# Optimization experiments

Measured on AMD Instinct MI355X. Metric: run time of the kernel, lower is better.

The kernel has to match this reference:

```python
import jax, jax.numpy as jnp
import numpy as np
from jax import lax

# mamba-130m-style config
B, L = 2, 1024          # batch, seq_len
D = 768                 # hidden_size
E = 1536                # intermediate (expand=2)
N = 16                  # ssm state size
R = 48                  # time_step_rank = ceil(D/16)
K = 4                   # conv kernel
NL = 4                  # num layers
NC = 5                  # num classes
EPS = 1e-5


def setup_inputs() -> dict:
    key = jax.random.key(0)
    ks = jax.random.split(key, 10)
    s = 0.02
    return {
        "x": jax.random.normal(ks[0], (B, L, 12), dtype=jnp.float32),
        "proj_w": jax.random.normal(ks[1], (D, 12)) * s,
        "proj_b": jnp.zeros((D,), jnp.float32),
        "norm_w": jnp.ones((NL, D), jnp.float32),
        "in_w": jax.random.normal(ks[2], (NL, 2 * E, D)) * s,
        "conv_w": jax.random.normal(ks[3], (NL, E, K)) * s,
        "conv_b": jnp.zeros((NL, E), jnp.float32),
        "xproj_w": jax.random.normal(ks[4], (NL, R + 2 * N, E)) * s,
        "dt_w": jax.random.normal(ks[5], (NL, E, R)) * s,
        "dt_b": jnp.full((NL, E), -4.0, jnp.float32),  # softplus(-4) ~ small dt
        "A_log": jnp.tile(jnp.log(jnp.arange(1, N + 1, dtype=jnp.float32))[None, None, :], (NL, E, 1)),
        "D_param": jnp.ones((NL, E), jnp.float32),
        "out_w": jax.random.normal(ks[6], (NL, D, E)) * s,
        "fnorm_w": jnp.ones((D,), jnp.float32),
        "cls_w": jax.random.normal(ks[7], (NC, D)) * s,
        "cls_b": jnp.zeros((NC,), jnp.float32),
    }


def _rmsnorm(x, w):
    var = jnp.mean(x * x, axis=-1, keepdims=True)
    return x * lax.rsqrt(var + EPS) * w


def _causal_conv(u, w, b):
    # u: [B,L,E], w: [E,K] depthwise causal conv, left-pad K-1
    up = jnp.pad(u, ((0, 0), (K - 1, 0), (0, 0)))
    y = b
    for k in range(K):
        y = y + w[:, k] * up[:, k:k + L, :]
    return y


def _selective_scan(u, dt, A, Bm, Cm, Dp):
    # u, dt: [B,L,E]; Bm, Cm: [B,L,N]; A: [E,N]; Dp: [E]
    def step(h, inp):
        u_t, dt_t, B_t, C_t = inp  # [B,E],[B,E],[B,N],[B,N]
        dA = jnp.exp(dt_t[:, :, None] * A)                      # [B,E,N]
        h = h * dA + dt_t[:, :, None] * B_t[:, None, :] * u_t[:, :, None]
        y = jnp.einsum('ben,bn->be', h, C_t)
        return h, y

    h0 = jnp.zeros((u.shape[0], E, N), u.dtype)
    _, ys = lax.scan(step, h0,
                     (u.transpose(1, 0, 2), dt.transpose(1, 0, 2),
                      Bm.transpose(1, 0, 2), Cm.transpose(1, 0, 2)))
    return ys.transpose(1, 0, 2) + u * Dp


def reference(x, proj_w, proj_b, norm_w, in_w, conv_w, conv_b, xproj_w,
              dt_w, dt_b, A_log, D_param, out_w, fnorm_w, cls_w, cls_b):
    h = x @ proj_w.T + proj_b                                     # [B,L,D]
    for i in range(NL):
        res = h
        hn = _rmsnorm(h, norm_w[i])
        proj = hn @ in_w[i].T                                     # [B,L,2E]
        u, gate = proj[..., :E], proj[..., E:]
        u = jax.nn.silu(_causal_conv(u, conv_w[i], conv_b[i]))    # [B,L,E]
        xdbc = u @ xproj_w[i].T                                   # [B,L,R+2N]
        dt_r = xdbc[..., :R]
        Bm = xdbc[..., R:R + N]
        Cm = xdbc[..., R + N:]
        dt = jax.nn.softplus(dt_r @ dt_w[i].T + dt_b[i])          # [B,L,E]
        A = -jnp.exp(A_log[i])                                    # [E,N]
        y = _selective_scan(u, dt, A, Bm, Cm, D_param[i])
        y = y * jax.nn.silu(gate)
        h = res + y @ out_w[i].T
    h = _rmsnorm(h, fnorm_w)
    pooled = jnp.mean(h, axis=1)                                  # AdaptiveAvgPool1d(1)
    return pooled @ cls_w.T + cls_b                               # [B,NC]
```

## Files before the change

kernel.cpp:

```cpp
#include <hip/hip_runtime.h>

constexpr int B_  = 2;
constexpr int L_  = 1024;
constexpr int D_  = 768;
constexpr int E_  = 1536;
constexpr int N_  = 16;
constexpr int R_  = 48;
constexpr int NL_ = 4;
constexpr int NC_ = 5;
constexpr int M_  = B_ * L_;
constexpr int E2_ = 2 * E_;
constexpr int XD_ = R_ + 2 * N_;
constexpr float EPS_ = 1e-5f;

constexpr int NCH_ = 16;
constexpr int CL_  = L_ / NCH_;
constexpr int KS_  = 8;
constexpr int PC_  = 64;

typedef __attribute__((ext_vector_type(8))) short bf16x8;
typedef __attribute__((ext_vector_type(4))) float f32x4;
typedef const __attribute__((address_space(1))) void* gas_t;
typedef __attribute__((address_space(3))) void* las_t;

__device__ __forceinline__ float sigm(float x) { return 1.0f / (1.0f + __expf(-x)); }
__device__ __forceinline__ float softplusf(float x) { return x > 20.0f ? x : log1pf(__expf(x)); }
__device__ __forceinline__ ushort f2b(float f) {
  union { float f; unsigned u; } v; v.f = f;
  unsigned r = (v.u + 0x7fffu + ((v.u >> 16) & 1u)) >> 16;
  return (ushort)r;
}
__device__ __forceinline__ float b2f(ushort u) {
  union { unsigned u; float f; } v; v.u = ((unsigned)u) << 16;
  return v.f;
}
__device__ __forceinline__ float b2f_lo(unsigned p) {
  union { unsigned u; float f; } v; v.u = p << 16;
  return v.f;
}
__device__ __forceinline__ float b2f_hi(unsigned p) {
  union { unsigned u; float f; } v; v.u = p & 0xffff0000u;
  return v.f;
}

template <int CTRL>
__device__ __forceinline__ float dpp_add(float x) {
  int yi = __builtin_amdgcn_update_dpp(0, __builtin_bit_cast(int, x), CTRL, 0xf, 0xf, false);
  return x + __builtin_bit_cast(float, yi);
}
__device__ __forceinline__ float row_sum16(float x) {
  x = dpp_add<0x121>(x);
  x = dpp_add<0x122>(x);
  x = dpp_add<0x124>(x);
  x = dpp_add<0x128>(x);
  return x;
}

__device__ __forceinline__ float block_sum(float v, float* sm) {
  #pragma unroll
  for (int o = 32; o > 0; o >>= 1) v += __shfl_xor(v, o);
  if ((threadIdx.x & 63) == 0) sm[threadIdx.x >> 6] = v;
  __syncthreads();
  return sm[0] + sm[1] + sm[2] + sm[3];
}

constexpr int WS1_ = NL_ * E2_ * D_;
constexpr int WS2_ = NL_ * D_ * E_;
constexpr int WS3_ = NL_ * XD_ * E_;
constexpr int WS4_ = NL_ * E_ * 64;
constexpr int WTOT_ = WS1_ + WS2_ + WS3_ + WS4_;
constexpr int WB_ = WTOT_ / 4 / 256;
__global__ __launch_bounds__(256) void k_wprep(const float* __restrict__ in_w, const float* __restrict__ out_w,
                                               const float* __restrict__ xw, const float* __restrict__ dw,
                                               const float* __restrict__ nw,
                                               ushort* __restrict__ in_wb, ushort* __restrict__ out_wb,
                                               ushort* __restrict__ xwb, ushort* __restrict__ dtwb,
                                               const float* __restrict__ x, const float* __restrict__ pw,
                                               const float* __restrict__ pb, float* __restrict__ h,
                                               ushort* __restrict__ hb, float* __restrict__ ssq) {
  if (blockIdx.x >= WB_) {
    __shared__ float xs[12];
    __shared__ float sm[4];
    int bx = blockIdx.x - WB_;
    int m = bx / 3;
    int d = (bx % 3) * 256 + threadIdx.x;
    if (threadIdx.x < 12) xs[threadIdx.x] = x[m * 12 + threadIdx.x];
    __syncthreads();
    float acc = pb[d];
    #pragma unroll
    for (int j = 0; j < 12; j++) acc = fmaf(xs[j], pw[d * 12 + j], acc);
    h[(size_t)m * D_ + d] = acc;
    hb[(size_t)m * D_ + d] = f2b(acc);
    float s = block_sum(acc * acc, sm);
    if (threadIdx.x == 0) atomicAdd(&ssq[m], s);
    return;
  }
  int i = (blockIdx.x * 256 + threadIdx.x) * 4;
  if (i < WS1_) {
    float4 v = *(const float4*)(in_w + i);
    int l = i / (E2_ * D_);
    int d = i % D_;
    float4 w = *(const float4*)(nw + l * D_ + d);
    *(ushort4*)(in_wb + i) = make_ushort4(f2b(v.x * w.x), f2b(v.y * w.y), f2b(v.z * w.z), f2b(v.w * w.w));
  } else if (i < WS1_ + WS2_) {
    int j = i - WS1_;
    float4 v = *(const float4*)(out_w + j);
    *(ushort4*)(out_wb + j) = make_ushort4(f2b(v.x), f2b(v.y), f2b(v.z), f2b(v.w));
  } else if (i < WS1_ + WS2_ + WS3_) {
    int j = i - WS1_ - WS2_;
    float4 v = *(const float4*)(xw + j);
    *(ushort4*)(xwb + j) = make_ushort4(f2b(v.x), f2b(v.y), f2b(v.z), f2b(v.w));
  } else {
    int j = i - WS1_ - WS2_ - WS3_;
    int k = j & 63, e = j >> 6;
    ushort4 o;
    o.x = (k + 0 < R_) ? f2b(dw[e * R_ + k + 0]) : (ushort)0;
    o.y = (k + 1 < R_) ? f2b(dw[e * R_ + k + 1]) : (ushort)0;
    o.z = (k + 2 < R_) ? f2b(dw[e * R_ + k + 2]) : (ushort)0;
    o.w = (k + 3 < R_) ? f2b(dw[e * R_ + k + 3]) : (ushort)0;
    *(ushort4*)(dtwb + j) = o;
  }
}

template <int BM, int BN, int MODE>
__global__ __launch_bounds__(256) void k_gemm_bf(const ushort* __restrict__ A, const ushort* __restrict__ Bw,
                                                 void* __restrict__ Cv, const float* __restrict__ res,
                                                 ushort* __restrict__ Cb, float* __restrict__ ssq,
                                                 int Kd, int Nd) {
  constexpr int AM = BM / 32, BNF = BN / 32;
  __shared__ ushort sA[BM * 32];
  __shared__ ushort sB[BN * 32];
  const int tid = threadIdx.x;
  const int wave = tid >> 6, lane = tid & 63;
  const int q = lane >> 4, r = lane & 15;
  const int wm = wave >> 1, wn = wave & 1;
  const int m0 = blockIdx.y * BM, n0 = blockIdx.x * BN;
  f32x4 acc[AM][BNF] = {};

  for (int k0 = 0; k0 < Kd; k0 += 32) {
    #pragma unroll
    for (int j = 0; j < BM / 64; j++) {
      int i = j * 256 + tid;
      const ushort* gp = A + (size_t)(m0 + (i >> 2)) * Kd + k0 + ((i & 3) << 3);
      __builtin_amdgcn_global_load_lds((gas_t)gp, (las_t)(sA + ((j * 256 + wave * 64) << 3)), 16, 0, 0);
    }
    #pragma unroll
    for (int j = 0; j < BN / 64; j++) {
      int i = j * 256 + tid;
      const ushort* gp = Bw + (size_t)(n0 + (i >> 2)) * Kd + k0 + ((i & 3) << 3);
      __builtin_amdgcn_global_load_lds((gas_t)gp, (las_t)(sB + ((j * 256 + wave * 64) << 3)), 16, 0, 0);
    }
    __syncthreads();
    bf16x8 af[AM], bfv[BNF];
    #pragma unroll
    for (int mi = 0; mi < AM; mi++)
      af[mi] = *(const bf16x8*)&sA[(wm * (BM / 2) + mi * 16 + r) * 32 + q * 8];
    #pragma unroll
    for (int nj = 0; nj < BNF; nj++)
      bfv[nj] = *(const bf16x8*)&sB[(wn * (BN / 2) + nj * 16 + r) * 32 + q * 8];
    #pragma unroll
    for (int mi = 0; mi < AM; mi++)
      #pragma unroll
      for (int nj = 0; nj < BNF; nj++)
        acc[mi][nj] = __builtin_amdgcn_mfma_f32_16x16x32_bf16(af[mi], bfv[nj], acc[mi][nj], 0, 0, 0);
    __syncthreads();
  }
  #pragma unroll
  for (int mi = 0; mi < AM; mi++) {
    #pragma unroll
    for (int rg = 0; rg < 4; rg++) {
      int row = m0 + wm * (BM / 2) + mi * 16 + q * 4 + rg;
      float rs = 0.0f, ssl = 0.0f;
      if (MODE == 4) rs = rsqrtf(res[row] * (1.0f / D_) + EPS_);
      #pragma unroll
      for (int nj = 0; nj < BNF; nj++) {
        int col = n0 + wn * (BN / 2) + nj * 16 + r;
        size_t off = (size_t)row * Nd + col;
        float v = acc[mi][nj][rg];
        if (MODE == 4) {
          ((ushort*)Cv)[off] = f2b(v * rs);
        } else if (MODE == 5) {
          v += res[off];
          ((float*)Cv)[off] = v;
          Cb[off] = f2b(v);
          ssl = fmaf(v, v, ssl);
        }
      }
      if (MODE == 5) {
        float sr = row_sum16(ssl);
        if (r == 0) atomicAdd(&ssq[row], sr);
      }
    }
  }
}

__global__ __launch_bounds__(256) void k_gemm_x(const ushort* __restrict__ A, const ushort* __restrict__ Bw,
                                                float* __restrict__ part) {
  __shared__ ushort sA[64 * 32];
  __shared__ ushort sB[80 * 32];
  const int tid = threadIdx.x;
  const int wave = tid >> 6, lane = tid & 63;
  const int q = lane >> 4, r = lane & 15;
  const int m0 = blockIdx.x * 64;
  const int kbeg = blockIdx.y * (E_ / KS_), kend = kbeg + E_ / KS_;
  f32x4 acc[5] = {};

  for (int k0 = kbeg; k0 < kend; k0 += 32) {
    {
      const ushort* gp = A + (size_t)(m0 + wave * 16 + (lane >> 2)) * E_ + k0 + ((lane & 3) << 3);
      __builtin_amdgcn_global_load_lds((gas_t)gp, (las_t)(sA + (wave << 9)), 16, 0, 0);
    }
    #pragma unroll
    for (int j = wave; j < 5; j += 4) {
      const ushort* gp = Bw + (size_t)(j * 16 + (lane >> 2)) * E_ + k0 + ((lane & 3) << 3);
      __builtin_amdgcn_global_load_lds((gas_t)gp, (las_t)(sB + (j << 9)), 16, 0, 0);
    }
    __syncthreads();
    bf16x8 af = *(const bf16x8*)&sA[(wave * 16 + r) * 32 + q * 8];
    #pragma unroll
    for (int nj = 0; nj < 5; nj++) {
      bf16x8 bfv = *(const bf16x8*)&sB[(nj * 16 + r) * 32 + q * 8];
      acc[nj] = __builtin_amdgcn_mfma_f32_16x16x32_bf16(af, bfv, acc[nj], 0, 0, 0);
    }
    __syncthreads();
  }
  float* pp = part + (size_t)blockIdx.y * M_ * XD_;
  #pragma unroll
  for (int nj = 0; nj < 5; nj++) {
    int col = nj * 16 + r;
    #pragma unroll
    for (int rg = 0; rg < 4; rg++) {
      int row = m0 + wave * 16 + q * 4 + rg;
      pp[(size_t)row * XD_ + col] = acc[nj][rg];
    }
  }
}

__global__ __launch_bounds__(256) void k_xfin(const float* __restrict__ part, float* __restrict__ xdbc,
                                              ushort* __restrict__ xb, float* __restrict__ ssq) {
  int i = blockIdx.x * 256 + threadIdx.x;
  if (i < M_) ssq[i] = 0.0f;
  int m = i / XD_, col = i - m * XD_;
  float s = 0.0f;
  #pragma unroll
  for (int ks = 0; ks < KS_; ks++) s += part[(size_t)ks * M_ * XD_ + i];
  xdbc[i] = s;
  if (col < R_) xb[(size_t)m * 64 + col] = f2b(s);
  else if (col < 64) xb[(size_t)m * 64 + col] = 0;
}

constexpr int TC_ = 4;
__global__ __launch_bounds__(384) void k_conv2(const ushort* __restrict__ proj, const float* __restrict__ cw,
                                               const float* __restrict__ cb, ushort* __restrict__ ub16,
                                               ushort* __restrict__ gb16) {
  int m0 = blockIdx.x * TC_;
  int t0 = m0 & (L_ - 1);
  int base = m0 - t0;
  int e4 = threadIdx.x * 4;
  float wv[4][4];
  #pragma unroll
  for (int j = 0; j < 4; j++) {
    float4 w = *(const float4*)(cw + (e4 + j) * 4);
    wv[j][0] = w.x; wv[j][1] = w.y; wv[j][2] = w.z; wv[j][3] = w.w;
  }
  float4 bb = *(const float4*)(cb + e4);
  float bbv[4] = {bb.x, bb.y, bb.z, bb.w};
  float win[4][4];
  #pragma unroll
  for (int s = 0; s < 3; s++) {
    int t = t0 - 3 + s;
    if (t >= 0) {
      uint2 p = *(const uint2*)(proj + (size_t)(base + t) * E2_ + e4);
      win[s][0] = b2f_lo(p.x); win[s][1] = b2f_hi(p.x);
      win[s][2] = b2f_lo(p.y); win[s][3] = b2f_hi(p.y);
    } else {
      win[s][0] = win[s][1] = win[s][2] = win[s][3] = 0.0f;
    }
  }
  #pragma unroll
  for (int j = 0; j < TC_; j++) {
    size_t m = (size_t)(m0 + j);
    uint2 p = *(const uint2*)(proj + m * E2_ + e4);
    win[3][0] = b2f_lo(p.x); win[3][1] = b2f_hi(p.x);
    win[3][2] = b2f_lo(p.y); win[3][3] = b2f_hi(p.y);
    float o[4];
    #pragma unroll
    for (int c = 0; c < 4; c++) {
      float a = bbv[c];
      a = fmaf(wv[c][0], win[0][c], a);
      a = fmaf(wv[c][1], win[1][c], a);
      a = fmaf(wv[c][2], win[2][c], a);
      a = fmaf(wv[c][3], win[3][c], a);
      o[c] = a * sigm(a);
    }
    uint2 uo;
    uo.x = (unsigned)f2b(o[0]) | ((unsigned)f2b(o[1]) << 16);
    uo.y = (unsigned)f2b(o[2]) | ((unsigned)f2b(o[3]) << 16);
    *(uint2*)(ub16 + m * E_ + e4) = uo;
    #pragma unroll
    for (int s = 0; s < 3; s++) {
      win[s][0] = win[s + 1][0]; win[s][1] = win[s + 1][1];
      win[s][2] = win[s + 1][2]; win[s][3] = win[s + 1][3];
    }
  }
  #pragma unroll
  for (int j = 0; j < TC_; j++) {
    size_t m = (size_t)(m0 + j);
    uint2 g = *(const uint2*)(proj + m * E2_ + E_ + e4);
    float g0 = b2f_lo(g.x), g1 = b2f_hi(g.x), g2 = b2f_lo(g.y), g3 = b2f_hi(g.y);
    g0 *= sigm(g0); g1 *= sigm(g1); g2 *= sigm(g2); g3 *= sigm(g3);
    uint2 go;
    go.x = (unsigned)f2b(g0) | ((unsigned)f2b(g1) << 16);
    go.y = (unsigned)f2b(g2) | ((unsigned)f2b(g3) << 16);
    *(uint2*)(gb16 + m * E_ + e4) = go;
  }
}

__global__ __launch_bounds__(256, 6) void k_scanA(const ushort* __restrict__ u, const ushort* __restrict__ xb,
                                                  const ushort* __restrict__ dtw, const float* __restrict__ dtb_p,
                                                  const float* __restrict__ xdbc, const float* __restrict__ A_log,
                                                  float* __restrict__ Pst, float* __restrict__ Sst) {
  __shared__ float s_dt[CL_][16];
  __shared__ float s_u [CL_][16];
  __shared__ float s_b [CL_][16];
  const int tid = threadIdx.x;
  const int e0 = blockIdx.x << 4;
  const int b  = blockIdx.y;
  const int c  = blockIdx.z;
  const int n  = tid & 15, el = tid >> 4;
  const int e  = e0 + el;
  const int wave = tid >> 6, lane = tid & 63;
  const int q = lane >> 4, r = lane & 15;
  const float A = -__expf(A_log[e * N_ + n]);
  const int t0 = c * CL_;
  const int mb = b * L_ + t0;

  f32x4 dacc = {};
  #pragma unroll
  for (int k0 = 0; k0 < 64; k0 += 32) {
    bf16x8 af = *(const bf16x8*)&xb[(size_t)(mb + wave * 16 + r) * 64 + k0 + q * 8];
    bf16x8 bfv = *(const bf16x8*)&dtw[(e0 + r) * 64 + k0 + q * 8];
    dacc = __builtin_amdgcn_mfma_f32_16x16x32_bf16(af, bfv, dacc, 0, 0, 0);
  }
  {
    float db = dtb_p[e0 + r];
    #pragma unroll
    for (int rg = 0; rg < 4; rg++)
      s_dt[wave * 16 + q * 4 + rg][r] = softplusf(dacc[rg] + db);
  }

  #pragma unroll
  for (int j = 0; j < 4; j++) {
    int t = j * 16 + el;
    s_u[t][n] = b2f(u[(size_t)(mb + t) * E_ + e0 + n]);
    int idx = j * 256 + tid;
    s_b[idx >> 4][idx & 15] = xdbc[(size_t)(mb + (idx >> 4)) * XD_ + R_ + (idx & 15)];
  }
  __syncthreads();

  float hs = 0.0f, pp = 1.0f;
  #pragma unroll 8
  for (int t = 0; t < CL_; t++) {
    float dtv = s_dt[t][el];
    float dA = __expf(dtv * A);
    hs = fmaf(hs, dA, dtv * s_u[t][el] * s_b[t][n]);
    pp *= dA;
  }
  size_t o = (((size_t)(b * NCH_ + c) * E_) + e) * N_ + n;
  Pst[o] = pp;
  Sst[o] = hs;
}

__global__ __launch_bounds__(256, 6) void k_scanC(const ushort* __restrict__ u, const ushort* __restrict__ xb,
                                                  const ushort* __restrict__ dtw, const float* __restrict__ dtb_p,
                                                  const float* __restrict__ xdbc, const ushort* __restrict__ gb,
                                                  const float* __restrict__ A_log, const float* __restrict__ Dp,
                                                  const float* __restrict__ Pst, const float* __restrict__ Sst,
                                                  ushort* __restrict__ y) {
  __shared__ float  s_dt[CL_][16];
  __shared__ float  s_u [CL_][16];
  __shared__ float2 s_bc[CL_][16];
  __shared__ float2 s_og[CL_][16];
  __shared__ ushort s_y [CL_][16];
  const int tid = threadIdx.x;
  const int e0 = blockIdx.x << 4;
  const int b  = blockIdx.y;
  const int c  = blockIdx.z;
  const int n  = tid & 15, el = tid >> 4;
  const int e  = e0 + el;
  const int wave = tid >> 6, lane = tid & 63;
  const int q = lane >> 4, r = lane & 15;
  const float A = -__expf(A_log[e * N_ + n]);
  const float Dv = Dp[e0 + n];
  const int t0 = c * CL_;
  const int mb = b * L_ + t0;

  f32x4 dacc = {};
  #pragma unroll
  for (int k0 = 0; k0 < 64; k0 += 32) {
    bf16x8 af = *(const bf16x8*)&xb[(size_t)(mb + wave * 16 + r) * 64 + k0 + q * 8];
    bf16x8 bfv = *(const bf16x8*)&dtw[(e0 + r) * 64 + k0 + q * 8];
    dacc = __builtin_amdgcn_mfma_f32_16x16x32_bf16(af, bfv, dacc, 0, 0, 0);
  }
  {
    float db = dtb_p[e0 + r];
    #pragma unroll
    for (int rg = 0; rg < 4; rg++)
      s_dt[wave * 16 + q * 4 + rg][r] = softplusf(dacc[rg] + db);
  }

  float r_bc[8];
  #pragma unroll
  for (int j = 0; j < 8; j++) {
    int idx = j * 256 + tid;
    r_bc[j] = xdbc[(size_t)(mb + (idx >> 5)) * XD_ + R_ + (idx & 31)];
  }

  float hs = 0.0f;
  if (c > 0) {
    float pv[NCH_ - 1], sv[NCH_ - 1];
    #pragma unroll
    for (int cc = 0; cc < NCH_ - 1; cc++) {
      int ci = cc < c ? cc : c - 1;
      size_t o = (((size_t)(b * NCH_ + ci) * E_) + e) * N_ + n;
      pv[cc] = Pst[o];
      sv[cc] = Sst[o];
    }
    #pragma unroll
    for (int cc = 0; cc < NCH_ - 1; cc++) {
      bool v = cc < c;
      hs = fmaf(v ? pv[cc] : 1.0f, hs, v ? sv[cc] : 0.0f);
    }
  }

  #pragma unroll
  for (int j = 0; j < 4; j++) {
    int t = j * 16 + el;
    float uf = b2f(u[(size_t)(mb + t) * E_ + e0 + n]);
    s_u[t][n] = uf;
    s_og[t][n] = make_float2(uf * Dv, b2f(gb[(size_t)(mb + t) * E_ + e0 + n]));
  }
  #pragma unroll
  for (int j = 0; j < 8; j++) {
    int idx = j * 256 + tid;
    int t = idx >> 5, col = idx & 31;
    ((float*)&s_bc[t][0])[((col & 15) << 1) + (col >> 4)] = r_bc[j];
  }
  __syncthreads();

  #pragma unroll 8
  for (int t = 0; t < CL_; t++) {
    float dtv = s_dt[t][el];
    float2 bc  = s_bc[t][n];
    float dA = __expf(dtv * A);
    hs = fmaf(hs, dA, dtv * s_u[t][el] * bc.x);
    float p = row_sum16(hs * bc.y);
    if (n == 0) {
      float2 og = s_og[t][el];
      s_y[t][el] = f2b((p + og.x) * og.y);
    }
  }
  __syncthreads();

  {
    int row = tid >> 2, seg = tid & 3;
    uint2 v = *(const uint2*)&s_y[row][seg * 4];
    *(uint2*)(y + (size_t)(mb + row) * E_ + e0 + seg * 4) = v;
  }
}

__global__ __launch_bounds__(256) void k_pool(const float* __restrict__ h, float* __restrict__ pooledP) {
  __shared__ float sm[4];
  const int pc = blockIdx.x, b = blockIdx.y;
  const int tid = threadIdx.x;
  const int t0 = pc * (L_ / PC_);
  float a0 = 0.0f, a1 = 0.0f, a2 = 0.0f;
  for (int rowi = 0; rowi < L_ / PC_; rowi++) {
    const float* hr = h + (size_t)(b * L_ + t0 + rowi) * D_;
    float v0 = hr[tid], v1 = hr[tid + 256], v2 = hr[tid + 512];
    float s = block_sum(v0 * v0 + v1 * v1 + v2 * v2, sm);
    float rs = rsqrtf(s * (1.0f / D_) + EPS_);
    a0 = fmaf(v0, rs, a0); a1 = fmaf(v1, rs, a1); a2 = fmaf(v2, rs, a2);
    __syncthreads();
  }
  float* pp = pooledP + ((size_t)pc * B_ + b) * D_;
  pp[tid] = a0; pp[tid + 256] = a1; pp[tid + 512] = a2;
}

__global__ __launch_bounds__(256) void k_logits(const float* __restrict__ pooledP, const float* __restrict__ fw,
                                                const float* __restrict__ cw, const float* __restrict__ cb,
                                                float* __restrict__ out) {
  __shared__ float sp[B_ * D_];
  int tid = threadIdx.x;
  for (int d = tid; d < B_ * D_; d += 256) {
    int b = d / D_, dd = d - b * D_;
    float pd = 0.0f;
    #pragma unroll 8
    for (int pc = 0; pc < PC_; pc++) pd += pooledP[((size_t)pc * B_ + b) * D_ + dd];
    sp[d] = pd * fw[dd] * (1.0f / L_);
  }
  __syncthreads();
  int wv = tid >> 6, ln = tid & 63;
  for (int p = wv; p < B_ * NC_; p += 4) {
    int b = p / NC_, c = p % NC_;
    float s = 0.0f;
    for (int d = ln; d < D_; d += 64) s = fmaf(sp[b * D_ + d], cw[c * D_ + d], s);
    #pragma unroll
    for (int o = 32; o > 0; o >>= 1) s += __shfl_xor(s, o);
    if (ln == 0) out[p] = s + cb[c];
  }
}

extern "C" void kernel_launch(void* const* d_in, const int* in_sizes, int n_in,
                              void* d_out, int out_size, void* d_ws, size_t ws_size,
                              hipStream_t stream) {
  const float* x       = (const float*)d_in[0];
  const float* proj_w  = (const float*)d_in[1];
  const float* proj_b  = (const float*)d_in[2];
  const float* norm_w  = (const float*)d_in[3];
  const float* in_w    = (const float*)d_in[4];
  const float* conv_w  = (const float*)d_in[5];
  const float* conv_b  = (const float*)d_in[6];
  const float* xproj_w = (const float*)d_in[7];
  const float* dt_w    = (const float*)d_in[8];
  const float* dt_b    = (const float*)d_in[9];
  const float* A_log   = (const float*)d_in[10];
  const float* D_param = (const float*)d_in[11];
  const float* out_w   = (const float*)d_in[12];
  const float* fnorm_w = (const float*)d_in[13];
  const float* cls_w   = (const float*)d_in[14];
  const float* cls_b   = (const float*)d_in[15];
  float* out = (float*)d_out;

  float* h      = (float*)d_ws;
  float* xdbc   = h + (size_t)M_ * D_;
  float* ssq    = xdbc + (size_t)M_ * XD_;
  float* pooledP = ssq + M_;
  float* Pst    = pooledP + (size_t)PC_ * B_ * D_;
  float* Sst    = Pst + (size_t)B_ * NCH_ * E_ * N_;
  float* xpart  = Sst + (size_t)B_ * NCH_ * E_ * N_;
  ushort* proj_bf = (ushort*)(xpart + (size_t)KS_ * M_ * XD_);
  ushort* hb_bf   = proj_bf + (size_t)M_ * E2_;
  ushort* y_bf    = hb_bf + (size_t)M_ * D_;
  ushort* ub_bf   = y_bf + (size_t)M_ * E_;
  ushort* g_bf    = ub_bf + (size_t)M_ * E_;
  ushort* xdbc_bf = g_bf + (size_t)M_ * E_;
  ushort* xwb     = xdbc_bf + (size_t)M_ * 64;
  ushort* dtwb    = xwb + (size_t)NL_ * XD_ * E_;
  ushort* in_wb   = dtwb + (size_t)NL_ * E_ * 64;
  ushort* out_wb  = in_wb + (size_t)NL_ * E2_ * D_;

  hipMemsetAsync(ssq, 0, M_ * sizeof(float), stream);
  k_wprep<<<WB_ + 3 * M_, 256, 0, stream>>>(in_w, out_w, xproj_w, dt_w, norm_w,
                                            in_wb, out_wb, xwb, dtwb,
                                            x, proj_w, proj_b, h, hb_bf, ssq);

  for (int i = 0; i < NL_; i++) {
    k_gemm_bf<128, 128, 4><<<dim3(E2_ / 128, M_ / 128), 256, 0, stream>>>(
        hb_bf, in_wb + (size_t)i * E2_ * D_, proj_bf, ssq, nullptr, nullptr, D_, E2_);
    k_conv2<<<M_ / TC_, 384, 0, stream>>>(proj_bf, conv_w + i * E_ * 4, conv_b + i * E_,
                                          ub_bf, g_bf);
    k_gemm_x<<<dim3(M_ / 64, KS_), 256, 0, stream>>>(ub_bf, xwb + (size_t)i * XD_ * E_, xpart);
    k_xfin<<<M_ * XD_ / 256, 256, 0, stream>>>(xpart, xdbc, xdbc_bf, ssq);
    k_scanA<<<dim3(E_ / 16, B_, NCH_), 256, 0, stream>>>(
        ub_bf, xdbc_bf, dtwb + (size_t)i * E_ * 64, dt_b + (size_t)i * E_, xdbc,
        A_log + (size_t)i * E_ * N_, Pst, Sst);
    k_scanC<<<dim3(E_ / 16, B_, NCH_), 256, 0, stream>>>(
        ub_bf, xdbc_bf, dtwb + (size_t)i * E_ * 64, dt_b + (size_t)i * E_, xdbc, g_bf,
        A_log + (size_t)i * E_ * N_, D_param + i * E_, Pst, Sst, y_bf);
    k_gemm_bf<64, 64, 5><<<dim3(D_ / 64, M_ / 64), 256, 0, stream>>>(
        y_bf, out_wb + (size_t)i * D_ * E_, h, h, hb_bf, ssq, E_, D_);
  }

  k_pool<<<dim3(PC_, B_), 256, 0, stream>>>(h, pooledP);
  k_logits<<<1, 256, 0, stream>>>(pooledP, fnorm_w, cls_w, cls_b, out);
}
```

Baseline: 679.6 us.

## Fuse chunked selective scan into one cooperative kernel with grid sync

```diff
diff --git a/kernel.cpp b/kernel.cpp
--- a/kernel.cpp
+++ b/kernel.cpp
@@ -1,4 +1,5 @@
 #include <hip/hip_runtime.h>
+#include <hip/hip_cooperative_groups.h>
 
 constexpr int B_  = 2;
 constexpr int L_  = 1024;
@@ -15,6 +16,9 @@
 
 constexpr int NCH_ = 16;
 constexpr int CL_  = L_ / NCH_;
+constexpr int NCC_ = 4;
+constexpr int CLC_ = L_ / NCC_;
+constexpr int SCBC_ = (E_ / 16) * B_ * NCC_;
 constexpr int KS_  = 8;
 constexpr int PC_  = 64;
 
@@ -316,6 +320,107 @@
   }
 }
 
+__global__ __launch_bounds__(256, 3) void k_scanCoop(const ushort* __restrict__ u, const ushort* __restrict__ gb,
+                                                     const ushort* __restrict__ xb, const ushort* __restrict__ dtw,
+                                                     const float* __restrict__ dtb_p, const float* __restrict__ xdbc,
+                                                     const float* __restrict__ A_log, const float* __restrict__ Dp,
+                                                     float* __restrict__ Pst, float* __restrict__ Sst,
+                                                     ushort* __restrict__ y) {
+  __shared__ float  s_dt[CLC_][16];
+  __shared__ ushort s_u [CLC_][16];
+  __shared__ ushort s_g [CLC_][16];
+  __shared__ ushort s_y [CLC_][16];
+  const int tid = threadIdx.x;
+  const int bid = blockIdx.x;
+  const int g2  = bid % (B_ * (E_ / 16));
+  const int c   = bid / (B_ * (E_ / 16));
+  const int b   = g2 / (E_ / 16);
+  const int eb  = g2 - b * (E_ / 16);
+  const int e0  = eb << 4;
+  const int n = tid & 15, el = tid >> 4;
+  const int e = e0 + el;
+  const int wave = tid >> 6, lane = tid & 63;
+  const int q = lane >> 4, r = lane & 15;
+  const float A = -__expf(A_log[e * N_ + n]);
+  const int mb = b * L_ + c * CLC_;
+
+  #pragma unroll
+  for (int k2 = 0; k2 < CLC_ / 64; k2++) {
+    int T0 = (wave + 4 * k2) * 16;
+    f32x4 dacc = {};
+    #pragma unroll
+    for (int k0 = 0; k0 < 64; k0 += 32) {
+      bf16x8 af  = *(const bf16x8*)&xb[(size_t)(mb + T0 + r) * 64 + k0 + q * 8];
+      bf16x8 bfv = *(const bf16x8*)&dtw[(e0 + r) * 64 + k0 + q * 8];
+      dacc = __builtin_amdgcn_mfma_f32_16x16x32_bf16(af, bfv, dacc, 0, 0, 0);
+    }
+    float db = dtb_p[e0 + r];
+    #pragma unroll
+    for (int rg = 0; rg < 4; rg++)
+      s_dt[T0 + q * 4 + rg][r] = softplusf(dacc[rg] + db);
+  }
+  #pragma unroll
+  for (int j = 0; j < CLC_ / 128; j++) {
+    int row = j * 128 + (tid >> 1), half = tid & 1;
+    size_t go = (size_t)(mb + row) * E_ + e0 + half * 8;
+    *(uint4*)&s_u[row][half * 8] = *(const uint4*)(u + go);
+    *(uint4*)&s_g[row][half * 8] = *(const uint4*)(gb + go);
+  }
+  __syncthreads();
+
+  const float* xgB = xdbc + (size_t)mb * XD_ + R_ + n;
+  float hs = 0.0f, sdt = 0.0f;
+  #pragma unroll 8
+  for (int t = 0; t < CLC_; t++) {
+    float dtv = s_dt[t][el];
+    float dA = __expf(dtv * A);
+    hs = fmaf(hs, dA, dtv * b2f(s_u[t][el]) * xgB[t * XD_]);
+    sdt += dtv;
+  }
+  const size_t o = (((size_t)(b * NCC_ + c) * E_) + e) * N_ + n;
+  __hip_atomic_store(&Pst[o], __expf(A * sdt), __ATOMIC_RELAXED, __HIP_MEMORY_SCOPE_AGENT);
+  __hip_atomic_store(&Sst[o], hs, __ATOMIC_RELAXED, __HIP_MEMORY_SCOPE_AGENT);
+
+  cooperative_groups::this_grid().sync();
+
+  float hin = 0.0f;
+  if (c > 0) {
+    float pv[NCC_ - 1], sv[NCC_ - 1];
+    #pragma unroll
+    for (int cc = 0; cc < NCC_ - 1; cc++) {
+      int ci = cc < c ? cc : c - 1;
+      size_t oc = (((size_t)(b * NCC_ + ci) * E_) + e) * N_ + n;
+      pv[cc] = __hip_atomic_load(&Pst[oc], __ATOMIC_RELAXED, __HIP_MEMORY_SCOPE_AGENT);
+      sv[cc] = __hip_atomic_load(&Sst[oc], __ATOMIC_RELAXED, __HIP_MEMORY_SCOPE_AGENT);
+    }
+    #pragma unroll
+    for (int cc = 0; cc < NCC_ - 1; cc++) {
+      bool v = cc < c;
+      hin = fmaf(v ? pv[cc] : 1.0f, hin, v ? sv[cc] : 0.0f);
+    }
+  }
+
+  const float Dv = Dp[e];
+  const float* xgC = xdbc + (size_t)mb * XD_ + R_ + 16 + n;
+  float h2 = hin;
+  #pragma unroll 8
+  for (int t = 0; t < CLC_; t++) {
+    float dtv = s_dt[t][el];
+    float dA = __expf(dtv * A);
+    float uf = b2f(s_u[t][el]);
+    h2 = fmaf(h2, dA, dtv * uf * xgB[t * XD_]);
+    float p = row_sum16(h2 * xgC[t * XD_]);
+    if (n == 0)
+      s_y[t][el] = f2b((p + uf * Dv) * b2f(s_g[t][el]));
+  }
+  __syncthreads();
+  #pragma unroll
+  for (int j = 0; j < CLC_ / 128; j++) {
+    int row = j * 128 + (tid >> 1), half = tid & 1;
+    *(uint4*)(y + (size_t)(mb + row) * E_ + e0 + half * 8) = *(const uint4*)&s_y[row][half * 8];
+  }
+}
+
 __global__ __launch_bounds__(256, 6) void k_scanA(const ushort* __restrict__ u, const ushort* __restrict__ xb,
                                                   const ushort* __restrict__ dtw, const float* __restrict__ dtb_p,
                                                   const float* __restrict__ xdbc, const float* __restrict__ A_log,
@@ -550,6 +655,10 @@
   ushort* in_wb   = dtwb + (size_t)NL_ * E_ * 64;
   ushort* out_wb  = in_wb + (size_t)NL_ * E2_ * D_;
 
+  int coop_nb = 0;
+  bool coop = (hipOccupancyMaxActiveBlocksPerMultiprocessor(&coop_nb, k_scanCoop, 256, 0)
+               == hipSuccess) && (coop_nb * 256 >= SCBC_);
+
   hipMemsetAsync(ssq, 0, M_ * sizeof(float), stream);
   k_wprep<<<WB_ + 3 * M_, 256, 0, stream>>>(in_w, out_w, xproj_w, dt_w, norm_w,
                                             in_wb, out_wb, xwb, dtwb,
@@ -562,12 +671,30 @@
                                           ub_bf, g_bf);
     k_gemm_x<<<dim3(M_ / 64, KS_), 256, 0, stream>>>(ub_bf, xwb + (size_t)i * XD_ * E_, xpart);
     k_xfin<<<M_ * XD_ / 256, 256, 0, stream>>>(xpart, xdbc, xdbc_bf, ssq);
-    k_scanA<<<dim3(E_ / 16, B_, NCH_), 256, 0, stream>>>(
-        ub_bf, xdbc_bf, dtwb + (size_t)i * E_ * 64, dt_b + (size_t)i * E_, xdbc,
-        A_log + (size_t)i * E_ * N_, Pst, Sst);
-    k_scanC<<<dim3(E_ / 16, B_, NCH_), 256, 0, stream>>>(
-        ub_bf, xdbc_bf, dtwb + (size_t)i * E_ * 64, dt_b + (size_t)i * E_, xdbc, g_bf,
-        A_log + (size_t)i * E_ * N_, D_param + i * E_, Pst, Sst, y_bf);
+
+    const ushort* a_u  = ub_bf;
+    const ushort* a_g  = g_bf;
+    const ushort* a_xb = xdbc_bf;
+    const ushort* a_dw = dtwb + (size_t)i * E_ * 64;
+    const float*  a_db = dt_b + (size_t)i * E_;
+    const float*  a_xd = xdbc;
+    const float*  a_al = A_log + (size_t)i * E_ * N_;
+    const float*  a_dp = D_param + (size_t)i * E_;
+    float* a_P = Pst;
+    float* a_S = Sst;
+    ushort* a_y = y_bf;
+    bool done = false;
+    if (coop) {
+      void* args[] = {&a_u, &a_g, &a_xb, &a_dw, &a_db, &a_xd, &a_al, &a_dp, &a_P, &a_S, &a_y};
+      hipError_t ce = hipLaunchCooperativeKernel(k_scanCoop, dim3(SCBC_), dim3(256), args, 0, stream);
+      if (ce == hipSuccess) done = true; else coop = false;
+    }
+    if (!done) {
+      k_scanA<<<dim3(E_ / 16, B_, NCH_), 256, 0, stream>>>(
+          ub_bf, xdbc_bf, a_dw, a_db, xdbc, a_al, Pst, Sst);
+      k_scanC<<<dim3(E_ / 16, B_, NCH_), 256, 0, stream>>>(
+          ub_bf, xdbc_bf, a_dw, a_db, xdbc, g_bf, a_al, a_dp, Pst, Sst, y_bf);
+    }
     k_gemm_bf<64, 64, 5><<<dim3(D_ / 64, M_ / 64), 256, 0, stream>>>(
         y_bf, out_wb + (size_t)i * D_ * E_, h, h, hb_bf, ssq, E_, D_);
   }
```

Result: slower. 1.214 ms (+78.6%).
